# Optimization experiments

Measured on AMD Instinct MI355X. Metric: run time of the kernel, lower is better.

The kernel has to match this reference:

```python
import jax, jax.numpy as jnp
import numpy as np

EPS = 1e-8


def setup_inputs() -> dict:
    key = jax.random.key(0)
    k1, k2 = jax.random.split(key)
    predict_pc = jax.random.normal(k1, (4, 3, 4096), dtype=jnp.float32)  # Bx3xM
    gt_pc = jax.random.normal(k2, (4, 3, 4096), dtype=jnp.float32)      # Bx3xN
    return {"predict_pc": predict_pc, "gt_pc": gt_pc}


def reference(predict_pc, gt_pc):
    # predict_pc: Bx3xM, gt_pc: Bx3xN ; k=1 nearest neighbor each direction
    p = jnp.transpose(predict_pc, (0, 2, 1))  # B,M,3
    g = jnp.transpose(gt_pc, (0, 2, 1))       # B,N,3
    p2 = jnp.sum(p * p, axis=-1)  # B,M
    g2 = jnp.sum(g * g, axis=-1)  # B,N
    # squared L2 pairwise distances, B,M,N (computed once, used both directions)
    d2 = p2[:, :, None] + g2[:, None, :] - 2.0 * jnp.einsum("bmd,bnd->bmn", p, g)
    idx_g = jnp.argmin(d2, axis=2)  # B,M : nearest gt for each predicted point
    idx_p = jnp.argmin(d2, axis=1)  # B,N : nearest predicted for each gt point
    nearest_g = jnp.take_along_axis(g, idx_g[:, :, None], axis=1)  # B,M,3
    nearest_p = jnp.take_along_axis(p, idx_p[:, :, None], axis=1)  # B,N,3
    # robust_norm: sqrt(sum over coord dim + 1e-8)
    fwd_elem = jnp.sqrt(jnp.sum((nearest_g - p) ** 2, axis=-1) + EPS)  # B,M
    bwd_elem = jnp.sqrt(jnp.sum((nearest_p - g) ** 2, axis=-1) + EPS)  # B,N
    return fwd_elem.mean() + bwd_elem.mean()
```

## Files before the change

### kernel.cpp

```cpp
#include <hip/hip_runtime.h>
#include <math.h>

#define BATCH 4
#define NPTS 4096
#define THREADS 256
#define P 8
#define SEGS 32
#define CSEG (NPTS / SEGS)
#define PTGRPS (NPTS / (THREADS * P))
#define PASS1_BLOCKS (2 * BATCH * PTGRPS * SEGS)
#define TOTAL_PTS (2 * BATCH * NPTS)
#define PASS2_BLOCKS 128

#define EPS 1e-8f
#define BIG 1e30f

#define PMIN_FLOATS (SEGS * TOTAL_PTS)

__global__ __launch_bounds__(THREADS) void chamfer_pass1(
    const float* __restrict__ pred, const float* __restrict__ gt,
    float* __restrict__ pmin, float* __restrict__ acc, int* __restrict__ ctr)
{
    __shared__ float4 lc[CSEG];

    if (blockIdx.x == 0 && threadIdx.x == 0) { acc[0] = 0.0f; ctr[0] = 0; }

    const int bid   = blockIdx.x;
    const int seg   = bid & (SEGS - 1);
    const int ptgrp = (bid >> 5) & (PTGRPS - 1);
    const int batch = (bid >> 6) & (BATCH - 1);
    const int dir   = bid >> 8;

    const float* pts  = (dir == 0) ? pred : gt;
    const float* cand = (dir == 0) ? gt   : pred;

    if (threadIdx.x < CSEG) {
        const float* cb = cand + (size_t)batch * 3 * NPTS + seg * CSEG;
        const float x = cb[threadIdx.x];
        const float y = cb[NPTS + threadIdx.x];
        const float z = cb[2 * NPTS + threadIdx.x];
        const float s = -0.5f * fmaf(x, x, fmaf(y, y, z * z));
        lc[threadIdx.x] = make_float4(x, y, z, s);
    }
    __syncthreads();

    const float* pb = pts + (size_t)batch * 3 * NPTS;
    const int pbase = ptgrp * (THREADS * P) + threadIdx.x;
    float px[P], py[P], pz[P], smax[P];
    #pragma unroll
    for (int k = 0; k < P; ++k) {
        const int i = pbase + k * THREADS;
        px[k] = pb[i];
        py[k] = pb[NPTS + i];
        pz[k] = pb[2 * NPTS + i];
        smax[k] = -BIG;
    }

    #pragma unroll 2
    for (int g = 0; g < CSEG / 4; ++g) {
        const float4 c0 = lc[4 * g + 0];
        const float4 c1 = lc[4 * g + 1];
        const float4 c2 = lc[4 * g + 2];
        const float4 c3 = lc[4 * g + 3];
        #pragma unroll
        for (int k = 0; k < P; ++k) {
            float t0 = fmaf(px[k], c0.x, fmaf(py[k], c0.y, fmaf(pz[k], c0.z, c0.w)));
            float t1 = fmaf(px[k], c1.x, fmaf(py[k], c1.y, fmaf(pz[k], c1.z, c1.w)));
            float t2 = fmaf(px[k], c2.x, fmaf(py[k], c2.y, fmaf(pz[k], c2.z, c2.w)));
            float t3 = fmaf(px[k], c3.x, fmaf(py[k], c3.y, fmaf(pz[k], c3.z, c3.w)));
            smax[k] = fmaxf(smax[k], fmaxf(fmaxf(t0, t1), fmaxf(t2, t3)));
        }
    }

    const int gp = dir * (BATCH * NPTS) + batch * NPTS + pbase;
    #pragma unroll
    for (int k = 0; k < P; ++k) {
        const float p2 = fmaf(px[k], px[k], fmaf(py[k], py[k], pz[k] * pz[k]));
        pmin[(size_t)seg * TOTAL_PTS + gp + k * THREADS] = fmaf(-2.0f, smax[k], p2);
    }
}

__global__ __launch_bounds__(THREADS) void chamfer_pass2(
    const float* __restrict__ pmin, float* __restrict__ acc, int* __restrict__ ctr,
    float* __restrict__ out)
{
    const int p = blockIdx.x * THREADS + threadIdx.x;
    float v = BIG;
    #pragma unroll
    for (int s = 0; s < SEGS; ++s)
        v = fminf(v, pmin[(size_t)s * TOTAL_PTS + p]);
    float r = sqrtf(fmaxf(v, 0.0f) + EPS);

    #pragma unroll
    for (int off = 32; off; off >>= 1) r += __shfl_down(r, off, 64);
    __shared__ float wsum[THREADS / 64];
    if ((threadIdx.x & 63) == 0) wsum[threadIdx.x >> 6] = r;
    __syncthreads();

    if (threadIdx.x == 0) {
        const float bs = (wsum[0] + wsum[1]) + (wsum[2] + wsum[3]);
        atomicAdd(acc, bs);
        __threadfence();
        const int t = atomicAdd(ctr, 1);
        if (t == PASS2_BLOCKS - 1) {
            __threadfence();
            const float total = atomicAdd(acc, 0.0f);
            out[0] = total * (1.0f / (float)(BATCH * NPTS));
        }
    }
}

extern "C" void kernel_launch(void* const* d_in, const int* in_sizes, int n_in,
                              void* d_out, int out_size, void* d_ws, size_t ws_size,
                              hipStream_t stream) {
    const float* pred = (const float*)d_in[0];
    const float* gt   = (const float*)d_in[1];
    float* out  = (float*)d_out;
    float* pmin = (float*)d_ws;
    float* acc  = pmin + PMIN_FLOATS;
    int*   ctr  = (int*)(acc + 1);

    chamfer_pass1<<<PASS1_BLOCKS, THREADS, 0, stream>>>(pred, gt, pmin, acc, ctr);
    chamfer_pass2<<<PASS2_BLOCKS, THREADS, 0, stream>>>(pmin, acc, ctr, out);
}
```

Measured before the change: 72.51 us.

## Prepack candidates into float4 buffer and read them directly instead of via LDS

```diff
diff --git a/kernel.cpp b/kernel.cpp
--- a/kernel.cpp
+++ b/kernel.cpp
@@ -5,44 +5,48 @@
 #define NPTS 4096
 #define THREADS 256
 #define P 8
-#define SEGS 32
+#define SEGS 64
 #define CSEG (NPTS / SEGS)
 #define PTGRPS (NPTS / (THREADS * P))
 #define PASS1_BLOCKS (2 * BATCH * PTGRPS * SEGS)
 #define TOTAL_PTS (2 * BATCH * NPTS)
 #define PASS2_BLOCKS 128
+#define PACK_BLOCKS (TOTAL_PTS / THREADS)
 
 #define EPS 1e-8f
 #define BIG 1e30f
 
-#define PMIN_FLOATS (SEGS * TOTAL_PTS)
+#define PMIN_FLOATS ((size_t)SEGS * TOTAL_PTS)
+
+__global__ __launch_bounds__(THREADS) void chamfer_pack(
+    const float* __restrict__ pred, const float* __restrict__ gt,
+    float4* __restrict__ packed, float* __restrict__ acc, int* __restrict__ ctr)
+{
+    if (blockIdx.x == 0 && threadIdx.x == 0) { acc[0] = 0.0f; ctr[0] = 0; }
+    const int i     = blockIdx.x * THREADS + threadIdx.x;
+    const int n     = i & (NPTS - 1);
+    const int batch = (i >> 12) & (BATCH - 1);
+    const int dir   = i >> 14;
+    const float* src = (dir == 0) ? gt : pred;
+    const float* cb  = src + (size_t)batch * 3 * NPTS;
+    const float x = cb[n];
+    const float y = cb[NPTS + n];
+    const float z = cb[2 * NPTS + n];
+    const float w = -0.5f * fmaf(x, x, fmaf(y, y, z * z));
+    packed[i] = make_float4(x, y, z, w);
+}
 
 __global__ __launch_bounds__(THREADS) void chamfer_pass1(
     const float* __restrict__ pred, const float* __restrict__ gt,
-    float* __restrict__ pmin, float* __restrict__ acc, int* __restrict__ ctr)
+    const float4* __restrict__ packed, float* __restrict__ pmin)
 {
-    __shared__ float4 lc[CSEG];
-
-    if (blockIdx.x == 0 && threadIdx.x == 0) { acc[0] = 0.0f; ctr[0] = 0; }
-
     const int bid   = blockIdx.x;
     const int seg   = bid & (SEGS - 1);
-    const int ptgrp = (bid >> 5) & (PTGRPS - 1);
-    const int batch = (bid >> 6) & (BATCH - 1);
-    const int dir   = bid >> 8;
+    const int ptgrp = (bid >> 6) & (PTGRPS - 1);
+    const int batch = (bid >> 7) & (BATCH - 1);
+    const int dir   = bid >> 9;
 
-    const float* pts  = (dir == 0) ? pred : gt;
-    const float* cand = (dir == 0) ? gt   : pred;
-
-    if (threadIdx.x < CSEG) {
-        const float* cb = cand + (size_t)batch * 3 * NPTS + seg * CSEG;
-        const float x = cb[threadIdx.x];
-        const float y = cb[NPTS + threadIdx.x];
-        const float z = cb[2 * NPTS + threadIdx.x];
-        const float s = -0.5f * fmaf(x, x, fmaf(y, y, z * z));
-        lc[threadIdx.x] = make_float4(x, y, z, s);
-    }
-    __syncthreads();
+    const float* pts = (dir == 0) ? pred : gt;
 
     const float* pb = pts + (size_t)batch * 3 * NPTS;
     const int pbase = ptgrp * (THREADS * P) + threadIdx.x;
@@ -56,12 +60,15 @@
         smax[k] = -BIG;
     }
 
-    #pragma unroll 2
+    const float4* __restrict__ cp =
+        packed + ((size_t)(dir * BATCH + batch) * NPTS + seg * CSEG);
+
+    #pragma unroll 4
     for (int g = 0; g < CSEG / 4; ++g) {
-        const float4 c0 = lc[4 * g + 0];
-        const float4 c1 = lc[4 * g + 1];
-        const float4 c2 = lc[4 * g + 2];
-        const float4 c3 = lc[4 * g + 3];
+        const float4 c0 = cp[4 * g + 0];
+        const float4 c1 = cp[4 * g + 1];
+        const float4 c2 = cp[4 * g + 2];
+        const float4 c3 = cp[4 * g + 3];
         #pragma unroll
         for (int k = 0; k < P; ++k) {
             float t0 = fmaf(px[k], c0.x, fmaf(py[k], c0.y, fmaf(pz[k], c0.z, c0.w)));
@@ -115,11 +122,13 @@
                               hipStream_t stream) {
     const float* pred = (const float*)d_in[0];
     const float* gt   = (const float*)d_in[1];
-    float* out  = (float*)d_out;
-    float* pmin = (float*)d_ws;
-    float* acc  = pmin + PMIN_FLOATS;
-    int*   ctr  = (int*)(acc + 1);
+    float*  out    = (float*)d_out;
+    float*  pmin   = (float*)d_ws;
+    float4* packed = (float4*)(pmin + PMIN_FLOATS);
+    float*  acc    = (float*)(packed + TOTAL_PTS);
+    int*    ctr    = (int*)(acc + 1);
 
-    chamfer_pass1<<<PASS1_BLOCKS, THREADS, 0, stream>>>(pred, gt, pmin, acc, ctr);
+    chamfer_pack <<<PACK_BLOCKS,  THREADS, 0, stream>>>(pred, gt, packed, acc, ctr);
+    chamfer_pass1<<<PASS1_BLOCKS, THREADS, 0, stream>>>(pred, gt, packed, pmin);
     chamfer_pass2<<<PASS2_BLOCKS, THREADS, 0, stream>>>(pmin, acc, ctr, out);
 }
```

Result: slower. 79.73 us (+10.0%).
